# Optimization experiments

Hardware: AMD Instinct MI355X
Metric: run time of the kernel (lower is better)

The kernel has to match this reference:

```python
import jax, jax.numpy as jnp
import numpy as np

N_NODES = 50000
N_EDGES = 800000
HID = 64
N_LAYERS = 3
N_GRAPHS = 64
NEG_SLOPE = 0.01  # nn.LeakyReLU default


def setup_inputs() -> dict:
    key = jax.random.key(0)
    ks = jax.random.split(key, 10)
    return {
        "x": jax.random.normal(ks[0], (N_NODES, HID), dtype=jnp.float32),
        "edge_attr": jax.random.normal(ks[1], (N_EDGES,), dtype=jnp.float32),
        "edge_w": jax.random.normal(ks[2], (N_LAYERS, 1, HID), dtype=jnp.float32) * 0.1,
        "edge_b": jax.random.normal(ks[3], (N_LAYERS, HID), dtype=jnp.float32) * 0.1,
        "node_w": jax.random.normal(ks[4], (N_LAYERS, 2 * HID, HID), dtype=jnp.float32) * 0.05,
        "node_b": jax.random.normal(ks[5], (N_LAYERS, HID), dtype=jnp.float32) * 0.1,
        "fc_w": jax.random.normal(ks[6], (HID, 1), dtype=jnp.float32) * 0.1,
        "fc_b": jax.random.normal(ks[7], (1,), dtype=jnp.float32) * 0.1,
        "edge_index": jax.random.randint(ks[8], (2, N_EDGES), 0, N_NODES, dtype=jnp.int32),
        "batch": jnp.sort(jax.random.randint(ks[9], (N_NODES,), 0, N_GRAPHS, dtype=jnp.int32)),
    }


def reference(x, edge_attr, edge_w, edge_b, node_w, node_b, fc_w, fc_b, edge_index, batch):
    src = edge_index[0]  # x_j gathered from source nodes
    dst = edge_index[1]  # aggregated into target nodes (aggr='add')
    ea = edge_attr.reshape(-1, 1)  # [E, 1]
    for l in range(N_LAYERS):
        edge_emb = ea @ edge_w[l] + edge_b[l]                       # [E, H] edge MLP
        msg = jnp.concatenate([x[src], edge_emb], axis=1)            # [E, 2H] message
        aggr = jax.ops.segment_sum(msg, dst, num_segments=N_NODES)   # [N, 2H] scatter-add
        x = jax.nn.relu(aggr @ node_w[l] + node_b[l])                # update: node MLP + ReLU
        x = jnp.where(x >= 0, x, NEG_SLOPE * x)                      # LeakyReLU (dropout=0)
    # global_mean_pool over batch assignment
    sums = jax.ops.segment_sum(x, batch, num_segments=N_GRAPHS)      # [G, H]
    counts = jax.ops.segment_sum(jnp.ones((x.shape[0], 1), x.dtype), batch, num_segments=N_GRAPHS)
    pooled = sums / jnp.maximum(counts, 1.0)
    return pooled @ fc_w + fc_b  # [G, 1]
```

## Files before the change

kernel.cpp:

```cpp
#include <hip/hip_runtime.h>

#define N_NODES 50000
#define N_EDGES 800000
#define HID 64
#define N_LAYERS 3
#define N_GRAPHS 64
#define MAXDEG 64
#define FIXS 4096.0f
#define NBUCK 196
#define CAP 8064
#define CAP2 1600
#define SCB 2048

typedef unsigned int u32;
typedef unsigned short ushort_t;
typedef short bf16x8 __attribute__((ext_vector_type(8)));
typedef float f32x4 __attribute__((ext_vector_type(4)));
typedef float f32x2 __attribute__((ext_vector_type(2)));

__device__ __forceinline__ ushort_t f2bf(float f) {
    unsigned int u = __builtin_bit_cast(unsigned int, f);
    unsigned int r = u + 0x7fffu + ((u >> 16) & 1u);
    return (ushort_t)(r >> 16);
}
__device__ __forceinline__ unsigned char f2fp8(float f) {
    u32 p = __builtin_amdgcn_cvt_pk_fp8_f32(f, f, 0u, false);
    return (unsigned char)(p & 0xFFu);
}

__global__ __launch_bounds__(256) void fused_front_kernel(
        const int* __restrict__ src, const int* __restrict__ dst,
        const float* __restrict__ ea, int* __restrict__ bucketCur,
        uint2* __restrict__ recs,
        const float* __restrict__ x_in, uint2* __restrict__ xf8,
        const int* __restrict__ batch, int* __restrict__ gstart,
        const float* __restrict__ edge_w, const float* __restrict__ edge_b,
        const float* __restrict__ node_w, float* __restrict__ uv,
        const float* __restrict__ fc_b, float* __restrict__ out,
        int scBlocks, int cvtBlocks, int gbBlocks) {
    __shared__ u32 hist[256], pfx[256], excl[256], baseL[256], limL[256];
    __shared__ uint2 stage[SCB];
    int t = threadIdx.x;
    int b = (int)blockIdx.x;
    if (b < scBlocks) {
        int b0 = b * SCB;
        int nE = N_EDGES - b0; if (nE > SCB) nE = SCB;
        hist[t] = 0;
        __syncthreads();
        for (int i = t; i < nE; i += 256)
            atomicAdd(&hist[(dst[b0 + i] >> 8) & 255], 1u);
        __syncthreads();
        pfx[t] = hist[t];
        __syncthreads();
        for (int off = 1; off < 256; off <<= 1) {
            u32 v = (t >= off) ? pfx[t - off] : 0u;
            __syncthreads();
            pfx[t] += v;
            __syncthreads();
        }
        u32 cntv = hist[t];
        u32 ex = pfx[t] - cntv;
        excl[t] = ex;
        u32 gbase = 0;
        if (cntv > 0 && t < NBUCK) {
            u32 start = (u32)atomicAdd(&bucketCur[t], (int)cntv);
            if (start + cntv > (u32)CAP) cntv = (start < (u32)CAP) ? (u32)CAP - start : 0u;
            gbase = (u32)t * CAP + start;
        }
        baseL[t] = gbase;
        limL[t]  = ex + cntv;
        hist[t]  = ex;
        __syncthreads();
        for (int i = t; i < nE; i += 256) {
            int e = b0 + i;
            int d = dst[e];
            int s = src[e];
            float fv = (ea[e] + 8.0f) * FIXS;
            fv = fminf(fmaxf(fv, 0.0f), 65535.0f);
            u32 fx = __float2uint_rn(fv);
            u32 idx = atomicAdd(&hist[(d >> 8) & 255], 1u);
            uint2 r; r.x = (u32)s | (fx << 16); r.y = (u32)d;
            if (idx < (u32)SCB) stage[idx] = r;
        }
        __syncthreads();
        for (int i = t; i < nE; i += 256) {
            uint2 r = stage[i];
            u32 bk = (r.y >> 8) & 255;
            if (bk < NBUCK && (u32)i < limL[bk])
                recs[(size_t)baseL[bk] + ((u32)i - excl[bk])] = r;
        }
        return;
    }
    if (b < scBlocks + cvtBlocks) {
        int i = (b - scBlocks) * 256 + t;
        if (i < N_NODES * HID / 8) {
            const float4* p = (const float4*)(x_in + (size_t)i * 8);
            float4 a = p[0], c = p[1];
            u32 lo = __builtin_amdgcn_cvt_pk_fp8_f32(a.x, a.y, 0u, false);
            lo      = __builtin_amdgcn_cvt_pk_fp8_f32(a.z, a.w, lo, true);
            u32 hi = __builtin_amdgcn_cvt_pk_fp8_f32(c.x, c.y, 0u, false);
            hi      = __builtin_amdgcn_cvt_pk_fp8_f32(c.z, c.w, hi, true);
            uint2 o; o.x = lo; o.y = hi;
            xf8[i] = o;
        }
        return;
    }
    if (b < scBlocks + cvtBlocks + gbBlocks) {
        int i = (b - scBlocks - cvtBlocks) * 256 + t;
        if (i >= N_NODES) return;
        int bi = batch[i];
        if (i == 0) {
            for (int g = 0; g <= bi; g++) gstart[g] = 0;
        } else {
            int bp = batch[i - 1];
            for (int g = bp + 1; g <= bi; g++) gstart[g] = i;
        }
        if (i == N_NODES - 1) {
            for (int g = bi + 1; g <= N_GRAPHS; g++) gstart[g] = N_NODES;
        }
        return;
    }
    if (t >= 192) {
        if (t < 192 + N_GRAPHS) out[t - 192] = fc_b[0];
        return;
    }
    int l = t >> 6, hp = t & 63;
    const float* w2 = node_w + l * 2 * HID * HID + HID * HID + hp;
    float u = 0.f, v = 0.f;
    for (int h = 0; h < HID; h++) {
        float w = w2[h * HID];
        u += edge_w[l * HID + h] * w;
        v += edge_b[l * HID + h] * w;
    }
    uv[l * 2 * HID + hp]       = u;
    uv[l * 2 * HID + HID + hp] = v;
}

__global__ __launch_bounds__(256) void build_ell_kernel(
        const uint2* __restrict__ recs, const int* __restrict__ bucketCur,
        u32* __restrict__ ell, int* __restrict__ cnt) {
    __shared__ u32 hist[64], pfx[64], excl[64];
    __shared__ u32 stagePay[CAP2];
    __shared__ ushort_t nodeOf[CAP2];
    int t = threadIdx.x;
    int b = blockIdx.x >> 2, sub = blockIdx.x & 3;
    size_t eBase = (size_t)b * CAP;
    int m = bucketCur[b];
    if (m > CAP) m = CAP;
    if (m < 0) m = 0;
    if (t < 64) hist[t] = 0;
    __syncthreads();
    for (int i = t; i < m; i += 256) {
        u32 y = recs[eBase + i].y;
        if ((int)((y >> 6) & 3) == sub) atomicAdd(&hist[y & 63], 1u);
    }
    __syncthreads();
    if (t < 64) pfx[t] = hist[t];
    __syncthreads();
    for (int off = 1; off < 64; off <<= 1) {
        u32 v = (t < 64 && t >= off) ? pfx[t - off] : 0u;
        __syncthreads();
        if (t < 64) pfx[t] += v;
        __syncthreads();
    }
    int node = b * 256 + sub * 64 + (t & 63);
    if (t < 64) {
        u32 full = hist[t];
        u32 ex = pfx[t] - full;
        excl[t] = ex;
        if (node < N_NODES) cnt[node] = (int)(full > MAXDEG ? MAXDEG : full);
        for (u32 r = 0; r < full && (ex + r) < (u32)CAP2; r++) nodeOf[ex + r] = (ushort_t)t;
        hist[t] = ex;
    }
    __syncthreads();
    int tot = (int)pfx[63];
    if (tot > CAP2) tot = CAP2;
    for (int i = t; i < m; i += 256) {
        uint2 r = recs[eBase + i];
        if ((int)((r.y >> 6) & 3) == sub) {
            u32 idx = atomicAdd(&hist[r.y & 63], 1u);
            if (idx < (u32)CAP2) stagePay[idx] = r.x;
        }
    }
    __syncthreads();
    for (int i = t; i < tot; i += 256) {
        u32 n64 = nodeOf[i];
        u32 rank = (u32)i - excl[n64];
        if (rank < MAXDEG)
            ell[((size_t)(b * 256 + sub * 64 + n64) << 6) + rank] = stagePay[i];
    }
}

__global__ __launch_bounds__(256) void agg_mfma_kernel(
        const unsigned char* __restrict__ xf8, const u32* __restrict__ ell,
        const int* __restrict__ cnt,
        const float* __restrict__ W1, const float* __restrict__ node_b_l,
        const float* __restrict__ uv_l, float* __restrict__ sattr,
        int layer0, unsigned char* __restrict__ out_f8, float* __restrict__ out_f32) {
    __shared__ float red[4][64][17];
    __shared__ u32   redS[4][16];
    int lane = threadIdx.x & 63;
    int w = threadIdx.x >> 6;
    int nodeBase = blockIdx.x * 16;
    int n16 = lane >> 2, q4 = lane & 3;

    int m = nodeBase + n16;
    int dg = cnt[m]; if (dg > MAXDEG) dg = MAXDEG;
    int mx = dg;
#pragma unroll
    for (int off = 4; off < 64; off <<= 1) {
        int o = __shfl_xor(mx, off);
        mx = o > mx ? o : mx;
    }

    const uint4* erow4 = (const uint4*)(ell + ((size_t)m << 6));
    const uint4* xq = (const uint4*)xf8;
    float acc[16];
#pragma unroll
    for (int j = 0; j < 16; j++) acc[j] = 0.f;
    u32 sfix = 0;
    int base = w * 4;
    uint4 e4 = {0, 0, 0, 0};
    if (base < mx) e4 = erow4[base >> 2];
    for (; base < mx; base += 16) {
        int nbase = base + 16;
        uint4 e4n = {0, 0, 0, 0};
        if (nbase < mx) e4n = erow4[nbase >> 2];
        u32 ee[4] = {e4.x, e4.y, e4.z, e4.w};
        uint4 rw[4];
        float f[4];
#pragma unroll
        for (int k = 0; k < 4; k++) {
            bool v = (base + k) < dg;
            sfix += (v && q4 == 0) ? (ee[k] >> 16) : 0u;
            int s = v ? (int)(ee[k] & 0xffffu) : 0;
            rw[k] = xq[(size_t)s * 4 + q4];
            f[k] = v ? 1.0f : 0.0f;
        }
#pragma unroll
        for (int k = 0; k < 4; k++) {
            u32 dw[4] = {rw[k].x, rw[k].y, rw[k].z, rw[k].w};
#pragma unroll
            for (int d0 = 0; d0 < 4; d0++) {
                f32x2 plo = __builtin_amdgcn_cvt_pk_f32_fp8(dw[d0], false);
                f32x2 phi = __builtin_amdgcn_cvt_pk_f32_fp8(dw[d0], true);
                acc[d0 * 4 + 0] += f[k] * plo[0];
                acc[d0 * 4 + 1] += f[k] * plo[1];
                acc[d0 * 4 + 2] += f[k] * phi[0];
                acc[d0 * 4 + 3] += f[k] * phi[1];
            }
        }
        e4 = e4n;
    }

#pragma unroll
    for (int j = 0; j < 16; j++) red[w][lane][j] = acc[j];
    if (q4 == 0) redS[w][n16] = sfix;
    __syncthreads();
    if (w != 0) return;

    int q = lane >> 4, n15 = lane & 15;
    float accA[8], accB[8];
#pragma unroll
    for (int j = 0; j < 8; j++) {
        int fA = 8 * q + j;
        int fB = 32 + 8 * q + j;
        int lA = n15 * 4 + (fA >> 4), eA = fA & 15;
        int lB = n15 * 4 + (fB >> 4), eB = fB & 15;
        accA[j] = red[0][lA][eA] + red[1][lA][eA] + red[2][lA][eA] + red[3][lA][eA];
        accB[j] = red[0][lB][eB] + red[1][lB][eB] + red[2][lB][eB] + red[3][lB][eB];
    }
    u32 sfix2 = redS[0][n15] + redS[1][n15] + redS[2][n15] + redS[3][n15];
    int m2 = nodeBase + n15;
    int dg2 = cnt[m2]; if (dg2 > MAXDEG) dg2 = MAXDEG;

    float satv;
    if (layer0) {
        satv = (float)(int)sfix2 * (1.0f / FIXS) - 8.0f * (float)dg2;
        if (lane < 16) sattr[m2] = satv;
    } else {
        satv = sattr[m2];
    }

    bf16x8 af0, af1;
#pragma unroll
    for (int j = 0; j < 8; j++) {
        af0[j] = (short)f2bf(accA[j]);
        af1[j] = (short)f2bf(accB[j]);
    }

    int q8 = q * 8;
    f32x4 c[4];
#pragma unroll
    for (int nt = 0; nt < 4; nt++) {
        bf16x8 b0, b1;
#pragma unroll
        for (int j = 0; j < 8; j++) {
            b0[j] = (short)f2bf(W1[(q8 + j) * HID + nt * 16 + n15]);
            b1[j] = (short)f2bf(W1[(32 + q8 + j) * HID + nt * 16 + n15]);
        }
        f32x4 z = {0.f, 0.f, 0.f, 0.f};
        c[nt] = __builtin_amdgcn_mfma_f32_16x16x32_bf16(af0, b0, z, 0, 0, 0);
        c[nt] = __builtin_amdgcn_mfma_f32_16x16x32_bf16(af1, b1, c[nt], 0, 0, 0);
    }

    float dgown = (float)dg2;
    float sat[4], dgf[4];
#pragma unroll
    for (int r = 0; r < 4; r++) {
        int srcLane = q * 4 + r;
        sat[r] = __shfl(satv, srcLane);
        dgf[r] = __shfl(dgown, srcLane);
    }
#pragma unroll
    for (int nt = 0; nt < 4; nt++) {
        int col = nt * 16 + n15;
        float uc = uv_l[col], vc = uv_l[HID + col], bc = node_b_l[col];
#pragma unroll
        for (int r = 0; r < 4; r++) {
            int n = nodeBase + q * 4 + r;
            float val = c[nt][r] + sat[r] * uc + dgf[r] * vc + bc;
            val = val > 0.f ? val : 0.f;
            if (out_f8) out_f8[(size_t)n * HID + col] = f2fp8(val);
            else        out_f32[(size_t)n * HID + col] = val;
        }
    }
}

__global__ __launch_bounds__(256) void pool_fc_kernel(
        const float* __restrict__ x, const int* __restrict__ gstart,
        const float* __restrict__ fc_w, float* __restrict__ out) {
    __shared__ float red[4][HID];
    int g = blockIdx.x >> 3, s8 = blockIdx.x & 7;
    int lane = threadIdx.x & 63, w = threadIdx.x >> 6;
    int s = gstart[g], e = gstart[g + 1];
    float acc = 0.f;
    int r = s + s8 * 4 + w;
    for (; r + 96 < e; r += 128) {
        float a0 = x[(size_t)(r     ) * HID + lane];
        float a1 = x[(size_t)(r + 32) * HID + lane];
        float a2 = x[(size_t)(r + 64) * HID + lane];
        float a3 = x[(size_t)(r + 96) * HID + lane];
        acc += a0 + a1 + a2 + a3;
    }
    for (; r < e; r += 32) acc += x[(size_t)r * HID + lane];
    red[w][lane] = acc;
    __syncthreads();
    if (w != 0) return;
    acc = red[0][lane] + red[1][lane] + red[2][lane] + red[3][lane];
    float dot = acc * fc_w[lane];
    for (int off = 32; off > 0; off >>= 1) dot += __shfl_down(dot, off);
    if (lane == 0) {
        float cntf = (float)(e - s);
        if (cntf < 1.f) cntf = 1.f;
        atomicAdd(&out[g], dot / cntf);
    }
}

extern "C" void kernel_launch(void* const* d_in, const int* in_sizes, int n_in,
                              void* d_out, int out_size, void* d_ws, size_t ws_size,
                              hipStream_t stream) {
    const float* x_in      = (const float*)d_in[0];
    const float* edge_attr = (const float*)d_in[1];
    const float* edge_w    = (const float*)d_in[2];
    const float* edge_b    = (const float*)d_in[3];
    const float* node_w    = (const float*)d_in[4];
    const float* node_b    = (const float*)d_in[5];
    const float* fc_w      = (const float*)d_in[6];
    const float* fc_b      = (const float*)d_in[7];
    const int*   edge_index= (const int*)d_in[8];
    const int*   batch     = (const int*)d_in[9];
    float* out = (float*)d_out;

    unsigned char* xf8_0 = (unsigned char*)d_ws;
    unsigned char* xf8_1 = xf8_0 + (size_t)N_NODES * HID;
    float*    xA    = (float*)(xf8_1 + (size_t)N_NODES * HID);
    uint2*    recs  = (uint2*)xA;
    u32*      ell   = (u32*)(xA + (size_t)N_NODES * HID);
    int*      cnt   = (int*)(ell + (size_t)N_NODES * MAXDEG);
    int*      gstart= cnt + N_NODES;
    float*    sattr = (float*)(gstart + N_GRAPHS + 1);
    float*    uv    = sattr + N_NODES;
    int*      bucketCur = (int*)(uv + N_LAYERS * 2 * HID);

    const int* src = edge_index;
    const int* dst = edge_index + N_EDGES;

    hipMemsetAsync(bucketCur, 0, NBUCK * sizeof(int), stream);

    const int SC  = (N_EDGES + SCB - 1) / SCB;
    const int CVT = (N_NODES * HID / 8 + 255) / 256;
    const int GB  = (N_NODES + 255) / 256;
    fused_front_kernel<<<SC + CVT + GB + 1, 256, 0, stream>>>(
        src, dst, edge_attr, bucketCur, recs,
        x_in, (uint2*)xf8_0, batch, gstart,
        edge_w, edge_b, node_w, uv, fc_b, out, SC, CVT, GB);

    build_ell_kernel<<<NBUCK * 4, 256, 0, stream>>>(recs, bucketCur, ell, cnt);

    const int AGG_BLOCKS = N_NODES / 16;
    agg_mfma_kernel<<<AGG_BLOCKS, 256, 0, stream>>>(
        xf8_0, ell, cnt, node_w, node_b, uv, sattr, 1, xf8_1, nullptr);
    agg_mfma_kernel<<<AGG_BLOCKS, 256, 0, stream>>>(
        xf8_1, ell, cnt, node_w + (size_t)2 * HID * HID, node_b + HID, uv + 2 * HID,
        sattr, 0, xf8_0, nullptr);
    agg_mfma_kernel<<<AGG_BLOCKS, 256, 0, stream>>>(
        xf8_0, ell, cnt, node_w + (size_t)4 * HID * HID, node_b + 2 * HID, uv + 4 * HID,
        sattr, 0, nullptr, xA);

    pool_fc_kernel<<<N_GRAPHS * 8, 256, 0, stream>>>(xA, gstart, fc_w, out);
}
```

Measured before the change: 179.2 us.

## Split per-warp edge ranges contiguously and distribute node MLP tiles across all warps

Each warp now owns a contiguous 16-edge chunk of the ELL row, loaded once as a uint4 per lane and broadcast via shuffles. The old version strided across chunks with a prefetch loop. In the epilogue, all four warps now run the reduction and each computes one 16-column MFMA tile of the node MLP, instead of warp 0 doing all four tiles while the others exit. This is meant to cut serial epilogue work and the per-iteration edge loads, at the cost of redundant LDS reduction reads in every warp. The edge loop now assumes a maximum degree of 64, which matches MAXDEG.

```diff
diff --git a/kernel.cpp b/kernel.cpp
--- a/kernel.cpp
+++ b/kernel.cpp
@@ -219,45 +219,50 @@
 #pragma unroll
     for (int j = 0; j < 16; j++) acc[j] = 0.f;
     u32 sfix = 0;
-    int base = w * 4;
-    uint4 e4 = {0, 0, 0, 0};
-    if (base < mx) e4 = erow4[base >> 2];
-    for (; base < mx; base += 16) {
-        int nbase = base + 16;
-        uint4 e4n = {0, 0, 0, 0};
-        if (nbase < mx) e4n = erow4[nbase >> 2];
-        u32 ee[4] = {e4.x, e4.y, e4.z, e4.w};
-        uint4 rw[4];
-        float f[4];
-#pragma unroll
-        for (int k = 0; k < 4; k++) {
-            bool v = (base + k) < dg;
-            sfix += (v && q4 == 0) ? (ee[k] >> 16) : 0u;
-            int s = v ? (int)(ee[k] & 0xffffu) : 0;
-            rw[k] = xq[(size_t)s * 4 + q4];
-            f[k] = v ? 1.0f : 0.0f;
-        }
-#pragma unroll
-        for (int k = 0; k < 4; k++) {
-            u32 dw[4] = {rw[k].x, rw[k].y, rw[k].z, rw[k].w};
-#pragma unroll
-            for (int d0 = 0; d0 < 4; d0++) {
-                f32x2 plo = __builtin_amdgcn_cvt_pk_f32_fp8(dw[d0], false);
-                f32x2 phi = __builtin_amdgcn_cvt_pk_f32_fp8(dw[d0], true);
-                acc[d0 * 4 + 0] += f[k] * plo[0];
-                acc[d0 * 4 + 1] += f[k] * plo[1];
-                acc[d0 * 4 + 2] += f[k] * phi[0];
-                acc[d0 * 4 + 3] += f[k] * phi[1];
+    int wbase = w * 16;
+    if (wbase < mx) {
+        uint4 e_all = erow4[w * 4 + q4];
+#pragma unroll
+        for (int j = 0; j < 4; j++) {
+            int sb = wbase + j * 4;
+            if (sb < mx) {
+                int srcL = n16 * 4 + j;
+                u32 ee[4];
+                ee[0] = (u32)__shfl((int)e_all.x, srcL);
+                ee[1] = (u32)__shfl((int)e_all.y, srcL);
+                ee[2] = (u32)__shfl((int)e_all.z, srcL);
+                ee[3] = (u32)__shfl((int)e_all.w, srcL);
+                uint4 rw[4];
+                float f[4];
+#pragma unroll
+                for (int k = 0; k < 4; k++) {
+                    bool v = (sb + k) < dg;
+                    sfix += (v && q4 == 0) ? (ee[k] >> 16) : 0u;
+                    int s = v ? (int)(ee[k] & 0xffffu) : 0;
+                    rw[k] = xq[(size_t)s * 4 + q4];
+                    f[k] = v ? 1.0f : 0.0f;
+                }
+#pragma unroll
+                for (int k = 0; k < 4; k++) {
+                    u32 dw[4] = {rw[k].x, rw[k].y, rw[k].z, rw[k].w};
+#pragma unroll
+                    for (int d0 = 0; d0 < 4; d0++) {
+                        f32x2 plo = __builtin_amdgcn_cvt_pk_f32_fp8(dw[d0], false);
+                        f32x2 phi = __builtin_amdgcn_cvt_pk_f32_fp8(dw[d0], true);
+                        acc[d0 * 4 + 0] += f[k] * plo[0];
+                        acc[d0 * 4 + 1] += f[k] * plo[1];
+                        acc[d0 * 4 + 2] += f[k] * phi[0];
+                        acc[d0 * 4 + 3] += f[k] * phi[1];
+                    }
+                }
             }
         }
-        e4 = e4n;
     }
 
 #pragma unroll
     for (int j = 0; j < 16; j++) red[w][lane][j] = acc[j];
     if (q4 == 0) redS[w][n16] = sfix;
     __syncthreads();
-    if (w != 0) return;
 
     int q = lane >> 4, n15 = lane & 15;
     float accA[8], accB[8];
@@ -277,7 +282,7 @@
     float satv;
     if (layer0) {
         satv = (float)(int)sfix2 * (1.0f / FIXS) - 8.0f * (float)dg2;
-        if (lane < 16) sattr[m2] = satv;
+        if (w == 0 && lane < 16) sattr[m2] = satv;
     } else {
         satv = sattr[m2];
     }
@@ -289,20 +294,17 @@
         af1[j] = (short)f2bf(accB[j]);
     }
 
+    int nt = w;
     int q8 = q * 8;
-    f32x4 c[4];
-#pragma unroll
-    for (int nt = 0; nt < 4; nt++) {
-        bf16x8 b0, b1;
-#pragma unroll
-        for (int j = 0; j < 8; j++) {
-            b0[j] = (short)f2bf(W1[(q8 + j) * HID + nt * 16 + n15]);
-            b1[j] = (short)f2bf(W1[(32 + q8 + j) * HID + nt * 16 + n15]);
-        }
-        f32x4 z = {0.f, 0.f, 0.f, 0.f};
-        c[nt] = __builtin_amdgcn_mfma_f32_16x16x32_bf16(af0, b0, z, 0, 0, 0);
-        c[nt] = __builtin_amdgcn_mfma_f32_16x16x32_bf16(af1, b1, c[nt], 0, 0, 0);
-    }
+    bf16x8 b0, b1;
+#pragma unroll
+    for (int j = 0; j < 8; j++) {
+        b0[j] = (short)f2bf(W1[(q8 + j) * HID + nt * 16 + n15]);
+        b1[j] = (short)f2bf(W1[(32 + q8 + j) * HID + nt * 16 + n15]);
+    }
+    f32x4 c = {0.f, 0.f, 0.f, 0.f};
+    c = __builtin_amdgcn_mfma_f32_16x16x32_bf16(af0, b0, c, 0, 0, 0);
+    c = __builtin_amdgcn_mfma_f32_16x16x32_bf16(af1, b1, c, 0, 0, 0);
 
     float dgown = (float)dg2;
     float sat[4], dgf[4];
@@ -312,18 +314,15 @@
         sat[r] = __shfl(satv, srcLane);
         dgf[r] = __shfl(dgown, srcLane);
     }
-#pragma unroll
-    for (int nt = 0; nt < 4; nt++) {
-        int col = nt * 16 + n15;
-        float uc = uv_l[col], vc = uv_l[HID + col], bc = node_b_l[col];
-#pragma unroll
-        for (int r = 0; r < 4; r++) {
-            int n = nodeBase + q * 4 + r;
-            float val = c[nt][r] + sat[r] * uc + dgf[r] * vc + bc;
-            val = val > 0.f ? val : 0.f;
-            if (out_f8) out_f8[(size_t)n * HID + col] = f2fp8(val);
-            else        out_f32[(size_t)n * HID + col] = val;
-        }
+    int col = nt * 16 + n15;
+    float uc = uv_l[col], vc = uv_l[HID + col], bc = node_b_l[col];
+#pragma unroll
+    for (int r = 0; r < 4; r++) {
+        int n = nodeBase + q * 4 + r;
+        float val = c[r] + sat[r] * uc + dgf[r] * vc + bc;
+        val = val > 0.f ? val : 0.f;
+        if (out_f8) out_f8[(size_t)n * HID + col] = f2fp8(val);
+        else        out_f32[(size_t)n * HID + col] = val;
     }
 }
 
```

New measurement: 207.2 us. +15.7%, slower.
